# Performance work log

Measured on AMD Instinct MI355X. Metric: run time of the kernel, lower is better.

Reference implementation:

```python
import jax, jax.numpy as jnp
import numpy as np

N = 10000      # nodes
E = 320000     # edges (avg degree 32)
D_IN = 128
D_H = 256
D_C = 32       # comm_dim
D_OUT = 64


def setup_inputs() -> dict:
    key = jax.random.key(0)
    ks = jax.random.split(key, 14)
    p = lambda k, shape: jax.random.normal(k, shape, jnp.float32) * 0.02
    return {
        "x": jax.random.normal(ks[0], (N, D_IN), jnp.float32),
        "edge_index": jax.random.randint(ks[1], (2, E), 0, N),
        "W_in": p(ks[2], (D_IN, D_H)), "b_in": jnp.zeros((D_H,), jnp.float32),
        "Wq": p(ks[3], (D_H, D_C)),   "bq": jnp.zeros((D_C,), jnp.float32),
        "Wk": p(ks[4], (D_H, D_C)),   "bk": jnp.zeros((D_C,), jnp.float32),
        "Wv": p(ks[5], (D_H, D_H)),   "bv": jnp.zeros((D_H,), jnp.float32),
        "W1": p(ks[6], (2 * D_H, D_H)), "b1": jnp.zeros((D_H,), jnp.float32),
        "W2": p(ks[7], (D_H, D_OUT)),  "b2": jnp.zeros((D_OUT,), jnp.float32),
    }


def reference(x, edge_index, W_in, b_in, Wq, bq, Wk, bk, Wv, bv, W1, b1, W2, b2):
    n = x.shape[0]
    h = x @ W_in + b_in                       # [N, D_H]
    q = h @ Wq + bq                           # [N, D_C]
    k = h @ Wk + bk                           # [N, D_C]
    v = h @ Wv + bv                           # [N, D_H]
    scores = (q @ k.T) / np.sqrt(q.shape[-1]).astype(np.float32)  # [N, N]
    # torch: zeros -> scatter 1 at edges -> masked_fill(==0, -inf);
    # edge positions keep value 1.0 ADDED to scores (faithful quirk).
    mask = jnp.full((n, n), -jnp.inf, jnp.float32)
    mask = mask.at[edge_index[0], edge_index[1]].set(1.0)
    w = jax.nn.softmax(scores + mask, axis=-1)
    w = jnp.nan_to_num(w, nan=0.0)            # rows with no edges -> all zeros
    comm = w @ v                              # [N, D_H]
    combined = jnp.concatenate([h, comm], axis=-1)  # [N, 2*D_H]
    return jax.nn.relu(combined @ W1 + b1) @ W2 + b2  # [N, D_OUT]
```

## Files before the change

### kernel.cpp

```cpp
#include <hip/hip_runtime.h>
#include <stdint.h>
#include <stddef.h>

constexpr int N_NODES = 10000;
constexpr int N_EDGES = 320000;
constexpr int DIM_IN  = 128;
constexpr int DIM_H   = 256;
constexpr int DIM_C   = 32;
constexpr int DIM_OUT = 64;
constexpr int DIM_QKV = DIM_C + DIM_C + DIM_H;
constexpr int DIM_QK  = 2 * DIM_C;
constexpr int DIM_CAT = 2 * DIM_H;
constexpr float SCALE = 0.17677669529663687f;
constexpr int MAXD = 192;
constexpr float VSCALE = 64.0f;

#if __has_builtin(__builtin_amdgcn_cvt_pk_f32_fp8) && __has_builtin(__builtin_amdgcn_cvt_pk_fp8_f32)
#define V_FP8 1
#else
#define V_FP8 0
#endif

constexpr size_t alignw(size_t w) { return (w + 15) & ~size_t(15); }
constexpr size_t OFF_DEG    = 0;
constexpr size_t OFF_COL    = alignw(OFF_DEG + N_NODES);
constexpr size_t OFF_QK     = alignw(OFF_COL + (size_t)N_NODES * MAXD);
constexpr size_t OFF_BQKV   = alignw(OFF_QK + (size_t)N_NODES * DIM_QK);
constexpr size_t OFF_VBF    = alignw(OFF_BQKV + DIM_QKV);
constexpr size_t OFF_XBF    = alignw(OFF_VBF + (size_t)N_NODES * DIM_H / 2);
constexpr size_t OFF_CATBF  = alignw(OFF_XBF + (size_t)N_NODES * DIM_IN / 2);
constexpr size_t OFF_ZBF    = alignw(OFF_CATBF + (size_t)N_NODES * DIM_CAT / 2);
constexpr size_t OFF_WINT   = alignw(OFF_ZBF + (size_t)N_NODES * DIM_H / 2);
constexpr size_t OFF_WQKVT  = alignw(OFF_WINT + (size_t)DIM_H * DIM_IN / 2);
constexpr size_t OFF_W1T    = alignw(OFF_WQKVT + (size_t)DIM_QKV * DIM_H / 2);
constexpr size_t OFF_W2T    = alignw(OFF_W1T + (size_t)DIM_H * DIM_CAT / 2);

typedef __attribute__((ext_vector_type(8))) short short8;
typedef __attribute__((ext_vector_type(4))) float floatx4;
typedef __attribute__((ext_vector_type(2))) float floatx2;

__device__ inline unsigned short f2bf(float f) {
    uint32_t u = __builtin_bit_cast(uint32_t, f);
    uint32_t r = (u + 0x7fffu + ((u >> 16) & 1u)) >> 16;
    return (unsigned short)r;
}
__device__ inline float bf2f_lo(uint32_t u) { return __builtin_bit_cast(float, u << 16); }
__device__ inline float bf2f_hi(uint32_t u) { return __builtin_bit_cast(float, u & 0xffff0000u); }

template <bool RELU, int MODE>
__global__ __launch_bounds__(256)
void mfma_gemm(const unsigned short* __restrict__ A, int lda,
               const unsigned short* __restrict__ Bt,
               const float* __restrict__ bias,
               float* __restrict__ Cf, unsigned short* __restrict__ Cb, int ldc,
               int M, int K)
{
    constexpr int BM = 128, BN = 64, PAD = 40;
    __shared__ short As[BM * PAD];
    __shared__ short Bs[BN * PAD];
    const int tid   = threadIdx.x;
    const int wave  = tid >> 6;
    const int lane  = tid & 63;
    const int quad  = lane >> 4;
    const int col16 = lane & 15;
    const int row0  = blockIdx.y * BM;
    const int col0  = blockIdx.x * BN;

    floatx4 acc[2][4] = {};

    const int sr = tid >> 2;
    const int sc = (tid & 3) * 8;

    for (int k0 = 0; k0 < K; k0 += 32) {
        #pragma unroll
        for (int i = 0; i < 2; ++i) {
            int r = sr + i * 64;
            int gr = row0 + r;
            short8 v = {};
            if (gr < M) v = *(const short8*)(A + (size_t)gr * lda + k0 + sc);
            *(short8*)(As + r * PAD + sc) = v;
        }
        {
            short8 v = *(const short8*)(Bt + (size_t)(col0 + sr) * K + k0 + sc);
            *(short8*)(Bs + sr * PAD + sc) = v;
        }
        __syncthreads();
        short8 a0 = *(const short8*)(As + (wave * 32 + col16) * PAD + quad * 8);
        short8 a1 = *(const short8*)(As + (wave * 32 + 16 + col16) * PAD + quad * 8);
        #pragma unroll
        for (int nf = 0; nf < 4; ++nf) {
            short8 b = *(const short8*)(Bs + (nf * 16 + col16) * PAD + quad * 8);
            acc[0][nf] = __builtin_amdgcn_mfma_f32_16x16x32_bf16(a0, b, acc[0][nf], 0, 0, 0);
            acc[1][nf] = __builtin_amdgcn_mfma_f32_16x16x32_bf16(a1, b, acc[1][nf], 0, 0, 0);
        }
        __syncthreads();
    }
    #pragma unroll
    for (int mf = 0; mf < 2; ++mf)
        #pragma unroll
        for (int r = 0; r < 4; ++r) {
            int gr = row0 + wave * 32 + mf * 16 + quad * 4 + r;
            if (gr >= M) continue;
            #pragma unroll
            for (int nf = 0; nf < 4; ++nf) {
                int gc = col0 + nf * 16 + col16;
                float v = acc[mf][nf][r] + bias[gc];
                if (RELU) v = fmaxf(v, 0.f);
                if (MODE == 2) {
                    if (gc < DIM_QK) {
                        Cf[(size_t)gr * DIM_QK + gc] = v;
                    } else {
#if V_FP8
                        int pk = __builtin_amdgcn_cvt_pk_fp8_f32(v * VSCALE, 0.f, 0, false);
                        ((unsigned char*)Cb)[(size_t)gr * DIM_H + (gc - DIM_QK)] =
                            (unsigned char)(pk & 0xff);
#else
                        Cb[(size_t)gr * DIM_H + (gc - DIM_QK)] = f2bf(v);
#endif
                    }
                } else if (MODE == 1) {
                    Cb[(size_t)gr * ldc + gc] = f2bf(v);
                } else {
                    Cf[(size_t)gr * ldc + gc] = v;
                }
            }
        }
}

__global__ void zero_deg(int* __restrict__ deg) {
    int i = blockIdx.x * blockDim.x + threadIdx.x;
    if (i < N_NODES) deg[i] = 0;
}

__global__ void prep_all(const float* __restrict__ x, const int* __restrict__ ei,
                         const float* __restrict__ W_in,
                         const float* __restrict__ Wq, const float* __restrict__ Wk,
                         const float* __restrict__ Wv,
                         const float* __restrict__ bq, const float* __restrict__ bk,
                         const float* __restrict__ bv,
                         const float* __restrict__ W1, const float* __restrict__ W2,
                         int* __restrict__ deg, int* __restrict__ col,
                         unsigned short* __restrict__ xb,
                         unsigned short* __restrict__ WinT, unsigned short* __restrict__ WqkvT,
                         unsigned short* __restrict__ W1T, unsigned short* __restrict__ W2T,
                         float* __restrict__ bqkv)
{
    int i = blockIdx.x * blockDim.x + threadIdx.x;
    int stride = gridDim.x * blockDim.x;
    for (int e = i; e < N_EDGES; e += stride) {
        int src = ei[e];
        int dst = ei[N_EDGES + e];
        int slot = atomicAdd(&deg[src], 1);
        if (slot < MAXD) col[src * MAXD + slot] = dst;
    }
    for (int idx = i; idx < (N_NODES * DIM_IN) / 8; idx += stride) {
        float4 a = ((const float4*)x)[2 * idx];
        float4 b = ((const float4*)x)[2 * idx + 1];
        uint4 o;
        o.x = (uint32_t)f2bf(a.x) | ((uint32_t)f2bf(a.y) << 16);
        o.y = (uint32_t)f2bf(a.z) | ((uint32_t)f2bf(a.w) << 16);
        o.z = (uint32_t)f2bf(b.x) | ((uint32_t)f2bf(b.y) << 16);
        o.w = (uint32_t)f2bf(b.z) | ((uint32_t)f2bf(b.w) << 16);
        ((uint4*)xb)[idx] = o;
    }
    for (int idx = i; idx < DIM_H * DIM_IN; idx += stride) {
        int n = idx / DIM_IN, k = idx % DIM_IN;
        WinT[idx] = f2bf(W_in[k * DIM_H + n]);
    }
    for (int idx = i; idx < DIM_QKV * DIM_H; idx += stride) {
        int n = idx / DIM_H, k = idx % DIM_H;
        float v = (n < DIM_C)     ? Wq[k * DIM_C + n]
                : (n < 2 * DIM_C) ? Wk[k * DIM_C + (n - DIM_C)]
                                  : Wv[k * DIM_H + (n - 2 * DIM_C)];
        WqkvT[idx] = f2bf(v);
    }
    for (int idx = i; idx < DIM_H * DIM_CAT; idx += stride) {
        int n = idx / DIM_CAT, k = idx % DIM_CAT;
        W1T[idx] = f2bf(W1[k * DIM_H + n]);
    }
    for (int idx = i; idx < DIM_OUT * DIM_H; idx += stride) {
        int n = idx / DIM_H, k = idx % DIM_H;
        W2T[idx] = f2bf(W2[k * DIM_OUT + n]);
    }
    for (int idx = i; idx < DIM_QKV; idx += stride)
        bqkv[idx] = (idx < DIM_C) ? bq[idx]
                  : (idx < 2 * DIM_C) ? bk[idx - DIM_C] : bv[idx - 2 * DIM_C];
}

__global__ __launch_bounds__(256)
void attn_row(const float* __restrict__ qk, const unsigned short* __restrict__ v_tab,
              const int* __restrict__ deg, const int* __restrict__ col,
              unsigned short* __restrict__ cat_bf) {
    __shared__ int   dstS[4][MAXD];
    __shared__ float wS[4][MAXD];
    __shared__ float qS[4][DIM_C];
    const int wave = threadIdx.x >> 6;
    const int lane = threadIdx.x & 63;
    const int row = blockIdx.x * 4 + wave;
    int d = deg[row];
    if (d > MAXD) d = MAXD;
    const int* crow = col + (size_t)row * MAXD;

    for (int p = lane; p < d; p += 64) dstS[wave][p] = crow[p];
    if (lane < DIM_C) qS[wave][lane] = qk[(size_t)row * DIM_QK + lane];
    __syncthreads();

    float mysum = 0.f;
    if (d <= 64) {
        int mydst = (lane < d) ? dstS[wave][lane] : -1;
        bool dup = false;
        #pragma unroll
        for (int k = 0; k < 63; ++k) {
            int other = __shfl(mydst, k, 64);
            dup = dup || (k < lane && other == mydst);
        }
        float w = 0.f;
        if (lane < d && !dup) {
            const float4* kp = (const float4*)(qk + (size_t)mydst * DIM_QK + DIM_C);
            float s = 0.f;
            #pragma unroll
            for (int i = 0; i < DIM_C / 4; ++i) {
                float4 b = kp[i];
                s += qS[wave][4 * i + 0] * b.x + qS[wave][4 * i + 1] * b.y
                   + qS[wave][4 * i + 2] * b.z + qS[wave][4 * i + 3] * b.w;
            }
            w = expf(s * SCALE);
        }
        wS[wave][lane] = w;
        mysum = w;
    } else {
        for (int p = lane; p < d; p += 64) {
            int mydst = dstS[wave][p];
            bool dup = false;
            for (int j = 0; j < p; ++j) dup = dup || (dstS[wave][j] == mydst);
            float w = 0.f;
            if (!dup) {
                const float4* kp = (const float4*)(qk + (size_t)mydst * DIM_QK + DIM_C);
                float s = 0.f;
                #pragma unroll
                for (int i = 0; i < DIM_C / 4; ++i) {
                    float4 b = kp[i];
                    s += qS[wave][4 * i + 0] * b.x + qS[wave][4 * i + 1] * b.y
                       + qS[wave][4 * i + 2] * b.z + qS[wave][4 * i + 3] * b.w;
                }
                w = expf(s * SCALE);
            }
            wS[wave][p] = w;
            mysum += w;
        }
    }
    #pragma unroll
    for (int off = 32; off; off >>= 1) mysum += __shfl_down(mysum, off, 64);
    float total = __shfl(mysum, 0, 64);
#if V_FP8
    float inv = (d > 0 && total > 0.f) ? 1.0f / (total * VSCALE) : 0.f;
#else
    float inv = (d > 0 && total > 0.f) ? 1.0f / total : 0.f;
#endif
    __syncthreads();

    float4 acc = make_float4(0.f, 0.f, 0.f, 0.f);
#if V_FP8
    const uint32_t* vb = (const uint32_t*)v_tab;
#else
    const uint2* vb = (const uint2*)v_tab;
#endif
    for (int p0 = 0; p0 < d; p0 += 16) {
        int j[16]; float w[16];
        #pragma unroll
        for (int t = 0; t < 16; ++t) {
            int idx = p0 + t;
            bool in = idx < d;
            j[t] = in ? dstS[wave][idx] : 0;
            w[t] = in ? wS[wave][idx] : 0.f;
        }
#if V_FP8
        uint32_t r[16];
        #pragma unroll
        for (int t = 0; t < 16; ++t) r[t] = vb[(size_t)j[t] * 64 + lane];
        #pragma unroll
        for (int t = 0; t < 16; ++t) {
            floatx2 lo = __builtin_amdgcn_cvt_pk_f32_fp8(r[t], false);
            floatx2 hi = __builtin_amdgcn_cvt_pk_f32_fp8(r[t], true);
            acc.x += w[t] * lo.x; acc.y += w[t] * lo.y;
            acc.z += w[t] * hi.x; acc.w += w[t] * hi.y;
        }
#else
        uint2 r[16];
        #pragma unroll
        for (int t = 0; t < 16; ++t) r[t] = vb[(size_t)j[t] * 64 + lane];
        #pragma unroll
        for (int t = 0; t < 16; ++t) {
            acc.x += w[t] * bf2f_lo(r[t].x);
            acc.y += w[t] * bf2f_hi(r[t].x);
            acc.z += w[t] * bf2f_lo(r[t].y);
            acc.w += w[t] * bf2f_hi(r[t].y);
        }
#endif
    }
    acc.x *= inv; acc.y *= inv; acc.z *= inv; acc.w *= inv;
    uint2 o;
    o.x = (uint32_t)f2bf(acc.x) | ((uint32_t)f2bf(acc.y) << 16);
    o.y = (uint32_t)f2bf(acc.z) | ((uint32_t)f2bf(acc.w) << 16);
    *(uint2*)(cat_bf + (size_t)row * DIM_CAT + DIM_H + lane * 4) = o;
}

extern "C" void kernel_launch(void* const* d_in, const int* in_sizes, int n_in,
                              void* d_out, int out_size, void* d_ws, size_t ws_size,
                              hipStream_t stream) {
    (void)in_sizes; (void)n_in; (void)out_size; (void)ws_size;
    const float* x    = (const float*)d_in[0];
    const int*   ei   = (const int*)d_in[1];
    const float* W_in = (const float*)d_in[2];
    const float* b_in = (const float*)d_in[3];
    const float* Wq   = (const float*)d_in[4];
    const float* bq   = (const float*)d_in[5];
    const float* Wk   = (const float*)d_in[6];
    const float* bk   = (const float*)d_in[7];
    const float* Wv   = (const float*)d_in[8];
    const float* bv   = (const float*)d_in[9];
    const float* W1   = (const float*)d_in[10];
    const float* b1   = (const float*)d_in[11];
    const float* W2   = (const float*)d_in[12];
    const float* b2   = (const float*)d_in[13];
    float* out = (float*)d_out;

    uint32_t* ws      = (uint32_t*)d_ws;
    int*      deg     = (int*)(ws + OFF_DEG);
    int*      col     = (int*)(ws + OFF_COL);
    float*    qk      = (float*)(ws + OFF_QK);
    float*    bqkv    = (float*)(ws + OFF_BQKV);
    unsigned short* v_tab  = (unsigned short*)(ws + OFF_VBF);
    unsigned short* x_bf   = (unsigned short*)(ws + OFF_XBF);
    unsigned short* cat_bf = (unsigned short*)(ws + OFF_CATBF);
    unsigned short* z_bf   = (unsigned short*)(ws + OFF_ZBF);
    unsigned short* WinT   = (unsigned short*)(ws + OFF_WINT);
    unsigned short* WqkvT  = (unsigned short*)(ws + OFF_WQKVT);
    unsigned short* W1T    = (unsigned short*)(ws + OFF_W1T);
    unsigned short* W2T    = (unsigned short*)(ws + OFF_W2T);

    zero_deg<<<(N_NODES + 255) / 256, 256, 0, stream>>>(deg);
    prep_all<<<640, 256, 0, stream>>>(x, ei, W_in, Wq, Wk, Wv, bq, bk, bv, W1, W2,
                                      deg, col, x_bf, WinT, WqkvT, W1T, W2T, bqkv);

    const int MB = (N_NODES + 127) / 128;
    mfma_gemm<false, 1><<<dim3(DIM_H / 64, MB), 256, 0, stream>>>(
        x_bf, DIM_IN, WinT, b_in, nullptr, cat_bf, DIM_CAT, N_NODES, DIM_IN);
    mfma_gemm<false, 2><<<dim3(DIM_QKV / 64, MB), 256, 0, stream>>>(
        cat_bf, DIM_CAT, WqkvT, bqkv, qk, v_tab, 0, N_NODES, DIM_H);
    attn_row<<<N_NODES / 4, 256, 0, stream>>>(qk, v_tab, deg, col, cat_bf);
    mfma_gemm<true, 1><<<dim3(DIM_H / 64, MB), 256, 0, stream>>>(
        cat_bf, DIM_CAT, W1T, b1, nullptr, z_bf, DIM_H, N_NODES, DIM_CAT);
    mfma_gemm<false, 0><<<dim3(DIM_OUT / 64, MB), 256, 0, stream>>>(
        z_bf, DIM_H, W2T, b2, out, nullptr, DIM_OUT, N_NODES, DIM_H);
}
```

Before: 179.5 us.

## Fuse W1 and W2 GEMMs into one kernel keeping hidden activations in LDS

Replaces the two back-to-back MFMA GEMMs (combined@W1 with ReLU, then @W2) with a single kernel. Each 64-row block computes the full 256-wide hidden tile, applies bias and ReLU, stores it as bf16 in shared memory reused from the B buffer, then multiplies by W2 read directly from global. This drops one kernel launch and the round trip of the z intermediate through global memory. In exchange the grid is smaller (157 blocks), each block holds 16 accumulators per thread, and W2 is read from global memory without LDS staging.

```diff
diff --git a/kernel.cpp b/kernel.cpp
--- a/kernel.cpp
+++ b/kernel.cpp
@@ -29,8 +29,7 @@
 constexpr size_t OFF_VBF    = alignw(OFF_BQKV + DIM_QKV);
 constexpr size_t OFF_XBF    = alignw(OFF_VBF + (size_t)N_NODES * DIM_H / 2);
 constexpr size_t OFF_CATBF  = alignw(OFF_XBF + (size_t)N_NODES * DIM_IN / 2);
-constexpr size_t OFF_ZBF    = alignw(OFF_CATBF + (size_t)N_NODES * DIM_CAT / 2);
-constexpr size_t OFF_WINT   = alignw(OFF_ZBF + (size_t)N_NODES * DIM_H / 2);
+constexpr size_t OFF_WINT   = alignw(OFF_CATBF + (size_t)N_NODES * DIM_CAT / 2);
 constexpr size_t OFF_WQKVT  = alignw(OFF_WINT + (size_t)DIM_H * DIM_IN / 2);
 constexpr size_t OFF_W1T    = alignw(OFF_WQKVT + (size_t)DIM_QKV * DIM_H / 2);
 constexpr size_t OFF_W2T    = alignw(OFF_W1T + (size_t)DIM_H * DIM_CAT / 2);
@@ -118,13 +117,89 @@
                         Cb[(size_t)gr * DIM_H + (gc - DIM_QK)] = f2bf(v);
 #endif
                     }
-                } else if (MODE == 1) {
+                } else {
                     Cb[(size_t)gr * ldc + gc] = f2bf(v);
-                } else {
-                    Cf[(size_t)gr * ldc + gc] = v;
                 }
             }
         }
+}
+
+__global__ __launch_bounds__(256)
+void gemm_w1w2(const unsigned short* __restrict__ cat, const unsigned short* __restrict__ W1T,
+               const float* __restrict__ b1, const unsigned short* __restrict__ W2T,
+               const float* __restrict__ b2, float* __restrict__ out, int M)
+{
+    constexpr int PAD = 40, TP = 260;
+    __shared__ short As[64 * PAD];
+    __shared__ short BsTs[64 * TP];
+    short* Bs = BsTs;
+    short* Ts = BsTs;
+    const int tid   = threadIdx.x;
+    const int wave  = tid >> 6;
+    const int lane  = tid & 63;
+    const int quad  = lane >> 4;
+    const int col16 = lane & 15;
+    const int row0  = blockIdx.x * 64;
+
+    const int sr = tid >> 2;
+    const int sc = (tid & 3) * 8;
+
+    floatx4 acc[16] = {};
+    for (int k0 = 0; k0 < DIM_CAT; k0 += 32) {
+        {
+            int gr = row0 + sr;
+            short8 v = {};
+            if (gr < M) v = *(const short8*)(cat + (size_t)gr * DIM_CAT + k0 + sc);
+            *(short8*)(As + sr * PAD + sc) = v;
+        }
+        #pragma unroll
+        for (int p = 0; p < 4; ++p) {
+            int r = sr + p * 64;
+            *(short8*)(Bs + r * PAD + sc) = *(const short8*)(W1T + (size_t)r * DIM_CAT + k0 + sc);
+        }
+        __syncthreads();
+        short8 a = *(const short8*)(As + (wave * 16 + col16) * PAD + quad * 8);
+        #pragma unroll
+        for (int nf = 0; nf < 16; ++nf) {
+            short8 b = *(const short8*)(Bs + (nf * 16 + col16) * PAD + quad * 8);
+            acc[nf] = __builtin_amdgcn_mfma_f32_16x16x32_bf16(a, b, acc[nf], 0, 0, 0);
+        }
+        __syncthreads();
+    }
+
+    #pragma unroll
+    for (int nf = 0; nf < 16; ++nf) {
+        int gc = nf * 16 + col16;
+        float bia = b1[gc];
+        #pragma unroll
+        for (int r = 0; r < 4; ++r) {
+            int lr = wave * 16 + quad * 4 + r;
+            float v = fmaxf(acc[nf][r] + bia, 0.f);
+            Ts[lr * TP + gc] = (short)f2bf(v);
+        }
+    }
+    __syncthreads();
+
+    floatx4 acc2[4] = {};
+    for (int k0 = 0; k0 < DIM_H; k0 += 32) {
+        short8 a = *(const short8*)(Ts + (wave * 16 + col16) * TP + k0 + quad * 8);
+        #pragma unroll
+        for (int nf = 0; nf < 4; ++nf) {
+            int brow = nf * 16 + col16;
+            short8 b = *(const short8*)(W2T + (size_t)brow * DIM_H + k0 + quad * 8);
+            acc2[nf] = __builtin_amdgcn_mfma_f32_16x16x32_bf16(a, b, acc2[nf], 0, 0, 0);
+        }
+    }
+    #pragma unroll
+    for (int nf = 0; nf < 4; ++nf) {
+        int gc = nf * 16 + col16;
+        float bia = b2[gc];
+        #pragma unroll
+        for (int r = 0; r < 4; ++r) {
+            int gr = row0 + wave * 16 + quad * 4 + r;
+            if (gr < M) out[(size_t)gr * DIM_OUT + gc] = acc2[nf][r] + bia;
+        }
+    }
 }
 
 __global__ void zero_deg(int* __restrict__ deg) {
@@ -333,7 +408,6 @@
     unsigned short* v_tab  = (unsigned short*)(ws + OFF_VBF);
     unsigned short* x_bf   = (unsigned short*)(ws + OFF_XBF);
     unsigned short* cat_bf = (unsigned short*)(ws + OFF_CATBF);
-    unsigned short* z_bf   = (unsigned short*)(ws + OFF_ZBF);
     unsigned short* WinT   = (unsigned short*)(ws + OFF_WINT);
     unsigned short* WqkvT  = (unsigned short*)(ws + OFF_WQKVT);
     unsigned short* W1T    = (unsigned short*)(ws + OFF_W1T);
@@ -349,8 +423,6 @@
     mfma_gemm<false, 2><<<dim3(DIM_QKV / 64, MB), 256, 0, stream>>>(
         cat_bf, DIM_CAT, WqkvT, bqkv, qk, v_tab, 0, N_NODES, DIM_H);
     attn_row<<<N_NODES / 4, 256, 0, stream>>>(qk, v_tab, deg, col, cat_bf);
-    mfma_gemm<true, 1><<<dim3(DIM_H / 64, MB), 256, 0, stream>>>(
-        cat_bf, DIM_CAT, W1T, b1, nullptr, z_bf, DIM_H, N_NODES, DIM_CAT);
-    mfma_gemm<false, 0><<<dim3(DIM_OUT / 64, MB), 256, 0, stream>>>(
-        z_bf, DIM_H, W2T, b2, out, nullptr, DIM_OUT, N_NODES, DIM_H);
-}
+    gemm_w1w2<<<(N_NODES + 63) / 64, 256, 0, stream>>>(
+        cat_bf, W1T, b1, W2T, b2, out, N_NODES);
+}
```

Measured after the change: 179.1 us (median of 2 runs). No clear change (-0.2%).
